# Optimization experiments

Hardware: AMD Instinct MI355X
Metric: run time of the kernel (lower is better)

Reference implementation:

```python
import jax, jax.numpy as jnp
import numpy as np

DIM = 2048
N_HEADS = 32
N_KV_HEADS = 4
HEAD_DIM = DIM // N_HEADS  # 64


def _rope_tables(T, head_dim, dtype):
    inv_freq = 1.0 / (10000.0 ** (jnp.arange(0, head_dim, 2, dtype=jnp.float32) / head_dim))
    t = jnp.arange(T, dtype=jnp.float32)
    freqs = jnp.einsum('i,j->ij', t, inv_freq)           # [T, head_dim/2]
    emb = jnp.concatenate([freqs, freqs], axis=-1)        # [T, head_dim]
    return jnp.cos(emb).astype(dtype), jnp.sin(emb).astype(dtype)


def _rotate_half(x):
    d = x.shape[-1] // 2
    return jnp.concatenate([-x[..., d:], x[..., :d]], axis=-1)


def setup_inputs() -> dict:
    key = jax.random.key(0)
    kx, kq, kk, kv, ko = jax.random.split(key, 5)
    s = 1.0 / np.sqrt(DIM)
    return {
        'x': jax.random.normal(kx, (2, 2048, DIM), dtype=jnp.float32),
        'wq': jax.random.normal(kq, (DIM, DIM), dtype=jnp.float32) * s,
        'wk': jax.random.normal(kk, (DIM, DIM // 8), dtype=jnp.float32) * s,
        'wv': jax.random.normal(kv, (DIM, DIM // 8), dtype=jnp.float32) * s,
        'wo': jax.random.normal(ko, (DIM, DIM), dtype=jnp.float32) * s,
    }


def reference(x, wq, wk, wv, wo):
    B, T, C = x.shape
    q = (x @ wq).reshape(B, T, N_HEADS, HEAD_DIM).transpose(0, 2, 1, 3)      # [B,H,T,D]
    k = (x @ wk).reshape(B, T, N_KV_HEADS, HEAD_DIM).transpose(0, 2, 1, 3)   # [B,Hkv,T,D]
    v = (x @ wv).reshape(B, T, N_KV_HEADS, HEAD_DIM).transpose(0, 2, 1, 3)

    cos, sin = _rope_tables(T, HEAD_DIM, x.dtype)  # [T,D]
    q = q * cos + _rotate_half(q) * sin
    k = k * cos + _rotate_half(k) * sin

    rep = N_HEADS // N_KV_HEADS
    k = jnp.repeat(k, rep, axis=1)  # [B,H,T,D]
    v = jnp.repeat(v, rep, axis=1)

    scale = 1.0 / np.sqrt(HEAD_DIM)
    scores = jnp.einsum('bhqd,bhkd->bhqk', q, k) * scale
    causal = jnp.tril(jnp.ones((T, T), dtype=bool))
    scores = jnp.where(causal, scores, jnp.finfo(scores.dtype).min)
    attn = jax.nn.softmax(scores, axis=-1)
    out = jnp.einsum('bhqk,bhkd->bhqd', attn, v)
    out = out.transpose(0, 2, 1, 3).reshape(B, T, C)
    return out @ wo
```

## Files before the change

kernel.cpp:

```cpp
#include <hip/hip_runtime.h>
#include <hip/hip_bf16.h>
#include <stdint.h>

#define DIM 2048
#define TSEQ 2048
#define BATCH 2
#define NH 32
#define NKV 4
#define HD 64
#define MROWS (BATCH*TSEQ)
#define NQKV 2560

typedef __attribute__((ext_vector_type(4))) float f32x4;
typedef __attribute__((ext_vector_type(8))) __bf16 bf16x8;
typedef unsigned short ushort_t;

#define GLDS16(g, l) __builtin_amdgcn_global_load_lds( \
    (const __attribute__((address_space(1))) void*)(g), \
    (__attribute__((address_space(3))) void*)(l), 16, 0, 0)

__device__ __forceinline__ float bflo2f(unsigned int w) {
  union { unsigned int i; float f; } c; c.i = w << 16; return c.f;
}
__device__ __forceinline__ unsigned short f2bf(float f) {
  union { float f; unsigned int i; } c; c.f = f;
  unsigned int x = c.i;
  x += 0x7fffu + ((x >> 16) & 1u);
  return (unsigned short)(x >> 16);
}
__device__ __forceinline__ unsigned short f2bf_fast(float f) {
  union { float f; unsigned int i; } c; c.f = f;
  return (unsigned short)((c.i + 0x8000u) >> 16);
}

__global__ void cast_bf16_k(const float* __restrict__ in, ushort_t* __restrict__ out, int n4) {
  const int i = blockIdx.x * 256 + threadIdx.x;
  if (i >= n4) return;
  const float4 v = ((const float4*)in)[i];
  uint2 p;
  p.x = (unsigned int)f2bf(v.x) | ((unsigned int)f2bf(v.y) << 16);
  p.y = (unsigned int)f2bf(v.z) | ((unsigned int)f2bf(v.w) << 16);
  ((uint2*)out)[i] = p;
}

__global__ void transpose_cast_all(const float* __restrict__ wq, const float* __restrict__ wk,
                                   const float* __restrict__ wv, const float* __restrict__ wo,
                                   ushort_t* __restrict__ wtq, ushort_t* __restrict__ woT) {
  __shared__ float tile[32][33];
  const int by = blockIdx.y;
  const float* src; ushort_t* dst; int N, bnb;
  if (by < 64)      { src = wq; dst = wtq;                    N = DIM; bnb = by; }
  else if (by < 72) { src = wk; dst = wtq + (long)DIM  * DIM; N = 256; bnb = by - 64; }
  else if (by < 80) { src = wv; dst = wtq + (long)2304 * DIM; N = 256; bnb = by - 72; }
  else              { src = wo; dst = woT;                    N = DIM; bnb = by - 80; }
  const int bk = blockIdx.x * 32;
  const int bn = bnb * 32;
  const int tx = threadIdx.x & 31;
  const int ty = threadIdx.x >> 5;
#pragma unroll
  for (int p = 0; p < 4; p++) {
    const int r = ty + p * 8;
    tile[r][tx] = src[(long)(bk + r) * N + bn + tx];
  }
  __syncthreads();
#pragma unroll
  for (int p = 0; p < 4; p++) {
    const int r = ty + p * 8;
    dst[(long)(bn + r) * DIM + bk + tx] = f2bf(tile[tx][r]);
  }
}

#define LOG1E4_D32 0.2878231366242557f
#define QSCALE 0.1803368801111243f

__global__ void rope_tab_k(float2* __restrict__ tab) {
  const int i = blockIdx.x * 256 + threadIdx.x;
  const int t = i >> 5, d = i & 31;
  const float ang = (float)t * __expf(-(float)d * LOG1E4_D32);
  float s_, c_;
  __sincosf(ang, &s_, &c_);
  tab[i] = make_float2(c_, s_);
}

template<int EPI>
__global__ __launch_bounds__(256, 4) void gemm_bt(
    const ushort_t* __restrict__ A, const ushort_t* __restrict__ BT,
    int M, int N, int K,
    float* __restrict__ Cf, ushort_t* __restrict__ Cq,
    ushort_t* __restrict__ Ck, ushort_t* __restrict__ Cv,
    const float2* __restrict__ tab)
{
  __shared__ __align__(16) ushort_t As[128][64];
  __shared__ __align__(16) ushort_t Bs[128][64];
  const int tid  = threadIdx.x;
  const int lane = tid & 63;
  const int wid  = tid >> 6;
  const int wm   = wid >> 1, wn = wid & 1;
  const int l8   = lane >> 3;
  const int c8   = (lane & 7) * 8;
  const long abase = (long)blockIdx.x * 128 * K;
  const long bbase = (long)blockIdx.y * 128 * K;
  const int rsel = lane & 15;
  const int koff = (lane >> 4) * 8;
  f32x4 acc[4][4] = {};

  for (int k0 = 0; k0 < K; k0 += 64) {
    __syncthreads();
#pragma unroll
    for (int i = 0; i < 4; i++) {
      const int r0 = wid * 32 + i * 8;
      GLDS16(&A [abase + (long)(r0 + l8) * K + k0 + c8], &As[r0][0]);
      GLDS16(&BT[bbase + (long)(r0 + l8) * K + k0 + c8], &Bs[r0][0]);
    }
    __syncthreads();
#pragma unroll
    for (int kk = 0; kk < 64; kk += 32) {
      bf16x8 af[4], bfr[4];
#pragma unroll
      for (int m = 0; m < 4; m++) af[m]  = *(const bf16x8*)(&As[wm*64 + m*16 + rsel][kk + koff]);
#pragma unroll
      for (int n = 0; n < 4; n++) bfr[n] = *(const bf16x8*)(&Bs[wn*64 + n*16 + rsel][kk + koff]);
#pragma unroll
      for (int m = 0; m < 4; m++)
#pragma unroll
        for (int n = 0; n < 4; n++)
          acc[m][n] = __builtin_amdgcn_mfma_f32_16x16x32_bf16(af[m], bfr[n], acc[m][n], 0, 0, 0);
    }
  }

  const int rbase = blockIdx.x * 128 + wm * 64 + (lane >> 4) * 4;
  const int l15e  = lane & 15;

  if (EPI == 1) {
    const int cbase = blockIdx.y * 128 + wn * 64 + l15e;
#pragma unroll
    for (int m = 0; m < 4; m++)
#pragma unroll
      for (int n = 0; n < 4; n++) {
        const int gn = cbase + n * 16;
#pragma unroll
        for (int j = 0; j < 4; j++)
          Cf[(long)(rbase + m * 16 + j) * N + gn] = acc[m][n][j];
      }
  } else {
    const int colbase = blockIdx.y * 128 + wn * 64;
    if (colbase >= DIM + 256) {
#pragma unroll
      for (int m = 0; m < 4; m++) {
        const int gm0 = rbase + m * 16;
        const int b = gm0 >> 11;
        const int t = gm0 & (TSEQ - 1);
#pragma unroll
        for (int n = 0; n < 4; n++) {
          const int x = colbase + n * 16 + l15e - DIM;
          const int hkv = (x >> 6) & 3;
          const int d = x & 63;
          uint2 pk;
          pk.x = (unsigned int)f2bf(acc[m][n][0]) | ((unsigned int)f2bf(acc[m][n][1]) << 16);
          pk.y = (unsigned int)f2bf(acc[m][n][2]) | ((unsigned int)f2bf(acc[m][n][3]) << 16);
          *(uint2*)(&Cv[((long)(b * NKV + hkv) * HD + d) * TSEQ + t]) = pk;
        }
      }
    } else {
      const bool isQ = (colbase < DIM);
      const int hkv = (colbase - DIM) >> 6;
#pragma unroll
      for (int m = 0; m < 4; m++) {
#pragma unroll
        for (int j = 0; j < 4; j++) {
          const int gm = rbase + m * 16 + j;
          const int t = gm & (TSEQ - 1);
          const int b = gm >> 11;
          const float2 cs0 = tab[t * 32 + l15e];
          const float2 cs1 = tab[t * 32 + 16 + l15e];
          const float v0 = acc[m][0][j], v1 = acc[m][1][j];
          const float v2 = acc[m][2][j], v3 = acc[m][3][j];
          const float r0 = v0 * cs0.x - v2 * cs0.y;
          const float r2 = v2 * cs0.x + v0 * cs0.y;
          const float r1 = v1 * cs1.x - v3 * cs1.y;
          const float r3 = v3 * cs1.x + v1 * cs1.y;
          if (isQ) {
            const long base = (long)gm * DIM + colbase + l15e;
            Cq[base]      = f2bf(r0 * QSCALE);
            Cq[base + 16] = f2bf(r1 * QSCALE);
            Cq[base + 32] = f2bf(r2 * QSCALE);
            Cq[base + 48] = f2bf(r3 * QSCALE);
          } else {
            const long base = ((long)(b * NKV + hkv) * TSEQ + t) * HD + l15e;
            Ck[base]      = f2bf(r0);
            Ck[base + 16] = f2bf(r1);
            Ck[base + 32] = f2bf(r2);
            Ck[base + 48] = f2bf(r3);
          }
        }
      }
    }
  }
}

__global__ __launch_bounds__(256, 4) void attn_mfma(
    const ushort_t* __restrict__ q, const ushort_t* __restrict__ k,
    const ushort_t* __restrict__ vt, ushort_t* __restrict__ o)
{
  __shared__ __align__(16) ushort_t Ks[2][64][64];
  __shared__ __align__(16) ushort_t Vs[2][64][64];

  const int tid  = threadIdx.x;
  const int lane = tid & 63;
  const int wid  = tid >> 6;
  const int l15  = lane & 15;
  const int lg   = lane >> 4;
  const int od   = lg & 1;
  const int hi   = lg >> 1;
  const int sw   = l15 & 7;

  const int bh  = blockIdx.x & 63;
  const int pq  = blockIdx.x >> 6;
  const int qtA = 31 - pq;
  const int qtB = pq;
  const int h   = bh & (NH - 1);
  const int b   = bh >> 5;
  const int hkv = h >> 3;
  const int qA0 = qtA * 64 + wid * 16;
  const int qB0 = qtB * 64 + wid * 16;

  bf16x8 qfA0, qfA1, qfB0, qfB1;
  {
    const ushort_t* qp = q + ((long)(b * TSEQ) + qA0 + l15) * DIM + h * 64 + lg * 8;
    qfA0 = *(const bf16x8*)(qp);
    qfA1 = *(const bf16x8*)(qp + 32);
    const ushort_t* qp2 = q + ((long)(b * TSEQ) + qB0 + l15) * DIM + h * 64 + lg * 8;
    qfB0 = *(const bf16x8*)(qp2);
    qfB1 = *(const bf16x8*)(qp2 + 32);
  }

  const ushort_t* kb_ = k  + (long)(b * NKV + hkv) * TSEQ * HD;
  const ushort_t* vb_ = vt + (long)(b * NKV + hkv) * HD * TSEQ;

  float lA = 0.f, lB = 0.f;
  f32x4 oA[4] = {}, oB[4] = {};

  const int srow = tid >> 2;
  const int sgc  = (tid & 3) * 16;
  const int g0   = 2 * (tid & 3);
  const int slc0 = ((g0    ) ^ (srow & 7)) * 8;
  const int slc1 = ((g0 + 1) ^ (srow & 7)) * 8;

  const int gv0 = ((0 + 2 * od + hi) ^ sw) * 8;
  const int gv1 = ((4 + 2 * od + hi) ^ sw) * 8;

  const int nkv = qtA + 1;

  *(uint4*)(&Ks[0][srow][slc0]) = *(const uint4*)(&kb_[(long)srow * HD + sgc]);
  *(uint4*)(&Ks[0][srow][slc1]) = *(const uint4*)(&kb_[(long)srow * HD + sgc + 8]);
  *(uint4*)(&Vs[0][srow][slc0]) = *(const uint4*)(&vb_[(long)srow * TSEQ + sgc]);
  *(uint4*)(&Vs[0][srow][slc1]) = *(const uint4*)(&vb_[(long)srow * TSEQ + sgc + 8]);
  int cur = 0;

#define PACK_KT(KT, UA, UB, LL) { \
    const float p0 = exp2f(st[KT][0]); \
    const float p1 = exp2f(st[KT][1]); \
    const float p2 = exp2f(st[KT][2]); \
    const float p3 = exp2f(st[KT][3]); \
    LL += (p0 + p1) + (p2 + p3); \
    asm("v_cvt_pk_bf16_f32 %0, %1, %2" : "=v"(UA) : "v"(p0), "v"(p1)); \
    asm("v_cvt_pk_bf16_f32 %0, %1, %2" : "=v"(UB) : "v"(p2), "v"(p3)); \
  }

#define PROC_TILE(QF0, QF1, OO, LL, Q0) \
  if (kb0 <= (Q0) + 15) { \
    f32x4 st[4] = {}; \
    __builtin_amdgcn_s_setprio(1); \
    _Pragma("unroll") \
    for (int kt = 0; kt < 4; kt++) { \
      const bf16x8 kf0 = *(const bf16x8*)(&Ks[cur][kt * 16 + l15][((0 + lg) ^ sw) * 8]); \
      st[kt] = __builtin_amdgcn_mfma_f32_16x16x32_bf16(kf0, QF0, st[kt], 0, 0, 0); \
      const bf16x8 kf1 = *(const bf16x8*)(&Ks[cur][kt * 16 + l15][((4 + lg) ^ sw) * 8]); \
      st[kt] = __builtin_amdgcn_mfma_f32_16x16x32_bf16(kf1, QF1, st[kt], 0, 0, 0); \
    } \
    __builtin_amdgcn_s_setprio(0); \
    if (kb0 + 63 > (Q0)) { \
      const int qg = (Q0) + l15; \
      _Pragma("unroll") \
      for (int kt = 0; kt < 4; kt++) { \
        const int kg0 = kb0 + kt * 16 + lg * 4; \
        _Pragma("unroll") \
        for (int j = 0; j < 4; j++) { \
          if (kg0 + j > qg) st[kt][j] = -1e30f; \
        } \
      } \
    } \
    unsigned int u00, u01, u10, u11, u20, u21, u30, u31; \
    PACK_KT(0, u00, u01, LL) \
    PACK_KT(1, u10, u11, LL) \
    PACK_KT(2, u20, u21, LL) \
    PACK_KT(3, u30, u31, LL) \
    const unsigned int r00 = __shfl_xor((int)(od ? u00 : u10), 16, 64); \
    const unsigned int r01 = __shfl_xor((int)(od ? u01 : u11), 16, 64); \
    const unsigned int r10 = __shfl_xor((int)(od ? u20 : u30), 16, 64); \
    const unsigned int r11 = __shfl_xor((int)(od ? u21 : u31), 16, 64); \
    union { unsigned int u[4]; bf16x8 v; } T0, T1; \
    T0.u[0] = od ? r00 : u00;  T0.u[1] = od ? r01 : u01; \
    T0.u[2] = od ? u10 : r00;  T0.u[3] = od ? u11 : r01; \
    T1.u[0] = od ? r10 : u20;  T1.u[1] = od ? r11 : u21; \
    T1.u[2] = od ? u30 : r10;  T1.u[3] = od ? u31 : r11; \
    __builtin_amdgcn_s_setprio(1); \
    _Pragma("unroll") \
    for (int nt = 0; nt < 4; nt++) { \
      const bf16x8 vf0 = *(const bf16x8*)(&Vs[cur][nt * 16 + l15][gv0]); \
      OO[nt] = __builtin_amdgcn_mfma_f32_16x16x32_bf16(T0.v, vf0, OO[nt], 0, 0, 0); \
    } \
    _Pragma("unroll") \
    for (int nt = 0; nt < 4; nt++) { \
      const bf16x8 vf1 = *(const bf16x8*)(&Vs[cur][nt * 16 + l15][gv1]); \
      OO[nt] = __builtin_amdgcn_mfma_f32_16x16x32_bf16(T1.v, vf1, OO[nt], 0, 0, 0); \
    } \
    __builtin_amdgcn_s_setprio(0); \
  }

  for (int kbv = 0; kbv < nkv; kbv++) {
    const int kb0 = kbv * 64;
    const bool pf = (kbv + 1 < nkv);
    uint4 kr0 = {}, kr1 = {}, vr0 = {}, vr1 = {};
    if (pf) {
      kr0 = *(const uint4*)(&kb_[(long)(kb0 + 64 + srow) * HD + sgc]);
      kr1 = *(const uint4*)(&kb_[(long)(kb0 + 64 + srow) * HD + sgc + 8]);
      vr0 = *(const uint4*)(&vb_[(long)srow * TSEQ + kb0 + 64 + sgc]);
      vr1 = *(const uint4*)(&vb_[(long)srow * TSEQ + kb0 + 64 + sgc + 8]);
    }
    asm volatile("s_waitcnt lgkmcnt(0)\n\ts_barrier" ::: "memory");

    PROC_TILE(qfA0, qfA1, oA, lA, qA0)
    PROC_TILE(qfB0, qfB1, oB, lB, qB0)

    if (pf) {
      *(uint4*)(&Ks[cur ^ 1][srow][slc0]) = kr0;
      *(uint4*)(&Ks[cur ^ 1][srow][slc1]) = kr1;
      *(uint4*)(&Vs[cur ^ 1][srow][slc0]) = vr0;
      *(uint4*)(&Vs[cur ^ 1][srow][slc1]) = vr1;
    }
    cur ^= 1;
  }
#undef PROC_TILE
#undef PACK_KT

  {
    float lc = lA;
    lc += __shfl_xor(lc, 16, 64);
    lc += __shfl_xor(lc, 32, 64);
    const long orow = (long)(b * TSEQ) + qA0;
#pragma unroll
    for (int j = 0; j < 4; j++) {
      const float inv = 1.f / __shfl(lc, (lane & 48) | (lg * 4 + j), 64);
#pragma unroll
      for (int nt = 0; nt < 4; nt++)
        o[(orow + lg * 4 + j) * DIM + h * 64 + nt * 16 + l15] = f2bf_fast(oA[nt][j] * inv);
    }
  }
  {
    float lc = lB;
    lc += __shfl_xor(lc, 16, 64);
    lc += __shfl_xor(lc, 32, 64);
    const long orow = (long)(b * TSEQ) + qB0;
#pragma unroll
    for (int j = 0; j < 4; j++) {
      const float inv = 1.f / __shfl(lc, (lane & 48) | (lg * 4 + j), 64);
#pragma unroll
      for (int nt = 0; nt < 4; nt++)
        o[(orow + lg * 4 + j) * DIM + h * 64 + nt * 16 + l15] = f2bf_fast(oB[nt][j] * inv);
    }
  }
}

extern "C" void kernel_launch(void* const* d_in, const int* in_sizes, int n_in,
                              void* d_out, int out_size, void* d_ws, size_t ws_size,
                              hipStream_t stream) {
  const float* x  = (const float*)d_in[0];
  const float* wq = (const float*)d_in[1];
  const float* wk = (const float*)d_in[2];
  const float* wv = (const float*)d_in[3];
  const float* wo = (const float*)d_in[4];
  float* out = (float*)d_out;

  ushort_t* ws = (ushort_t*)d_ws;
  const long NXB = (long)MROWS * DIM;
  ushort_t* xb   = ws;
  ushort_t* wtq  = xb  + NXB;
  ushort_t* woT  = wtq + (long)NQKV * DIM;
  ushort_t* qws  = woT + (long)DIM * DIM;
  ushort_t* kws  = qws + NXB;
  ushort_t* vtws = kws + (long)BATCH * NKV * TSEQ * HD;
  ushort_t* aws  = vtws + (long)BATCH * NKV * TSEQ * HD;
  float2*   tab  = (float2*)(aws + NXB);

  cast_bf16_k<<<(int)(NXB / 1024), 256, 0, stream>>>(x, xb, (int)(NXB / 4));
  transpose_cast_all<<<dim3(64, 144), 256, 0, stream>>>(wq, wk, wv, wo, wtq, woT);
  rope_tab_k<<<256, 256, 0, stream>>>(tab);

  gemm_bt<0><<<dim3(32, 20), 256, 0, stream>>>(xb, wtq, MROWS, NQKV, DIM,
                                               nullptr, qws, kws, vtws, tab);

  attn_mfma<<<BATCH * NH * 16, 256, 0, stream>>>(qws, kws, vtws, aws);

  gemm_bt<1><<<dim3(32, 16), 256, 0, stream>>>(aws, woT, MROWS, DIM, DIM,
                                               out, nullptr, nullptr, nullptr, nullptr);
}
```

Baseline: 203.3 us.

## Give each attention block one contiguous 128-row query tile so K/V fragments are shared

Each attention block now handles a single contiguous 128-row query tile, with each wave owning 32 consecutive rows, instead of pairing two 64-row tiles from opposite ends of the sequence. K and V fragments are loaded once from LDS into registers and reused for both 16-row halves of the wave, which halves LDS reads per MFMA. The K-loop now also skips fully masked tiles at the block level. The cost is higher register pressure, so launch bounds drop from 4 to 3 blocks per CU, and causal load balancing across blocks becomes uneven, now only mitigated by launching the longest tiles first.

```diff
diff --git a/kernel.cpp b/kernel.cpp
--- a/kernel.cpp
+++ b/kernel.cpp
@@ -198,7 +198,7 @@
   }
 }
 
-__global__ __launch_bounds__(256, 4) void attn_mfma(
+__global__ __launch_bounds__(256, 3) void attn_mfma(
     const ushort_t* __restrict__ q, const ushort_t* __restrict__ k,
     const ushort_t* __restrict__ vt, ushort_t* __restrict__ o)
 {
@@ -215,30 +215,27 @@
   const int sw   = l15 & 7;
 
   const int bh  = blockIdx.x & 63;
-  const int pq  = blockIdx.x >> 6;
-  const int qtA = 31 - pq;
-  const int qtB = pq;
+  const int qt  = (TSEQ / 128 - 1) - (blockIdx.x >> 6);
   const int h   = bh & (NH - 1);
   const int b   = bh >> 5;
   const int hkv = h >> 3;
-  const int qA0 = qtA * 64 + wid * 16;
-  const int qB0 = qtB * 64 + wid * 16;
-
-  bf16x8 qfA0, qfA1, qfB0, qfB1;
+  const int qw0 = qt * 128 + wid * 32;
+
+  bf16x8 qf0c0, qf0c1, qf1c0, qf1c1;
   {
-    const ushort_t* qp = q + ((long)(b * TSEQ) + qA0 + l15) * DIM + h * 64 + lg * 8;
-    qfA0 = *(const bf16x8*)(qp);
-    qfA1 = *(const bf16x8*)(qp + 32);
-    const ushort_t* qp2 = q + ((long)(b * TSEQ) + qB0 + l15) * DIM + h * 64 + lg * 8;
-    qfB0 = *(const bf16x8*)(qp2);
-    qfB1 = *(const bf16x8*)(qp2 + 32);
+    const ushort_t* qp0 = q + ((long)(b * TSEQ) + qw0 + l15) * DIM + h * 64 + lg * 8;
+    qf0c0 = *(const bf16x8*)(qp0);
+    qf0c1 = *(const bf16x8*)(qp0 + 32);
+    const ushort_t* qp1 = qp0 + 16 * DIM;
+    qf1c0 = *(const bf16x8*)(qp1);
+    qf1c1 = *(const bf16x8*)(qp1 + 32);
   }
 
   const ushort_t* kb_ = k  + (long)(b * NKV + hkv) * TSEQ * HD;
   const ushort_t* vb_ = vt + (long)(b * NKV + hkv) * HD * TSEQ;
 
-  float lA = 0.f, lB = 0.f;
-  f32x4 oA[4] = {}, oB[4] = {};
+  float lH0 = 0.f, lH1 = 0.f;
+  f32x4 oH0[4] = {}, oH1[4] = {};
 
   const int srow = tid >> 2;
   const int sgc  = (tid & 3) * 16;
@@ -249,7 +246,7 @@
   const int gv0 = ((0 + 2 * od + hi) ^ sw) * 8;
   const int gv1 = ((4 + 2 * od + hi) ^ sw) * 8;
 
-  const int nkv = qtA + 1;
+  const int nkv = 2 * qt + 2;
 
   *(uint4*)(&Ks[0][srow][slc0]) = *(const uint4*)(&kb_[(long)srow * HD + sgc]);
   *(uint4*)(&Ks[0][srow][slc1]) = *(const uint4*)(&kb_[(long)srow * HD + sgc + 8]);
@@ -257,65 +254,44 @@
   *(uint4*)(&Vs[0][srow][slc1]) = *(const uint4*)(&vb_[(long)srow * TSEQ + sgc + 8]);
   int cur = 0;
 
-#define PACK_KT(KT, UA, UB, LL) { \
-    const float p0 = exp2f(st[KT][0]); \
-    const float p1 = exp2f(st[KT][1]); \
-    const float p2 = exp2f(st[KT][2]); \
-    const float p3 = exp2f(st[KT][3]); \
+  union packu { unsigned int u[4]; bf16x8 v; };
+
+#define PK(ST, KT, UA, UB, LL) { \
+    const float p0 = exp2f(ST[KT][0]); \
+    const float p1 = exp2f(ST[KT][1]); \
+    const float p2 = exp2f(ST[KT][2]); \
+    const float p3 = exp2f(ST[KT][3]); \
     LL += (p0 + p1) + (p2 + p3); \
     asm("v_cvt_pk_bf16_f32 %0, %1, %2" : "=v"(UA) : "v"(p0), "v"(p1)); \
     asm("v_cvt_pk_bf16_f32 %0, %1, %2" : "=v"(UB) : "v"(p2), "v"(p3)); \
   }
 
-#define PROC_TILE(QF0, QF1, OO, LL, Q0) \
-  if (kb0 <= (Q0) + 15) { \
-    f32x4 st[4] = {}; \
-    __builtin_amdgcn_s_setprio(1); \
-    _Pragma("unroll") \
-    for (int kt = 0; kt < 4; kt++) { \
-      const bf16x8 kf0 = *(const bf16x8*)(&Ks[cur][kt * 16 + l15][((0 + lg) ^ sw) * 8]); \
-      st[kt] = __builtin_amdgcn_mfma_f32_16x16x32_bf16(kf0, QF0, st[kt], 0, 0, 0); \
-      const bf16x8 kf1 = *(const bf16x8*)(&Ks[cur][kt * 16 + l15][((4 + lg) ^ sw) * 8]); \
-      st[kt] = __builtin_amdgcn_mfma_f32_16x16x32_bf16(kf1, QF1, st[kt], 0, 0, 0); \
-    } \
-    __builtin_amdgcn_s_setprio(0); \
-    if (kb0 + 63 > (Q0)) { \
-      const int qg = (Q0) + l15; \
-      _Pragma("unroll") \
-      for (int kt = 0; kt < 4; kt++) { \
-        const int kg0 = kb0 + kt * 16 + lg * 4; \
-        _Pragma("unroll") \
-        for (int j = 0; j < 4; j++) { \
-          if (kg0 + j > qg) st[kt][j] = -1e30f; \
-        } \
-      } \
-    } \
+#define PACK_HALF(ST, LL, TT0, TT1) { \
     unsigned int u00, u01, u10, u11, u20, u21, u30, u31; \
-    PACK_KT(0, u00, u01, LL) \
-    PACK_KT(1, u10, u11, LL) \
-    PACK_KT(2, u20, u21, LL) \
-    PACK_KT(3, u30, u31, LL) \
+    PK(ST, 0, u00, u01, LL) \
+    PK(ST, 1, u10, u11, LL) \
+    PK(ST, 2, u20, u21, LL) \
+    PK(ST, 3, u30, u31, LL) \
     const unsigned int r00 = __shfl_xor((int)(od ? u00 : u10), 16, 64); \
     const unsigned int r01 = __shfl_xor((int)(od ? u01 : u11), 16, 64); \
     const unsigned int r10 = __shfl_xor((int)(od ? u20 : u30), 16, 64); \
     const unsigned int r11 = __shfl_xor((int)(od ? u21 : u31), 16, 64); \
-    union { unsigned int u[4]; bf16x8 v; } T0, T1; \
-    T0.u[0] = od ? r00 : u00;  T0.u[1] = od ? r01 : u01; \
-    T0.u[2] = od ? u10 : r00;  T0.u[3] = od ? u11 : r01; \
-    T1.u[0] = od ? r10 : u20;  T1.u[1] = od ? r11 : u21; \
-    T1.u[2] = od ? u30 : r10;  T1.u[3] = od ? u31 : r11; \
-    __builtin_amdgcn_s_setprio(1); \
+    TT0.u[0] = od ? r00 : u00;  TT0.u[1] = od ? r01 : u01; \
+    TT0.u[2] = od ? u10 : r00;  TT0.u[3] = od ? u11 : r01; \
+    TT1.u[0] = od ? r10 : u20;  TT1.u[1] = od ? r11 : u21; \
+    TT1.u[2] = od ? u30 : r10;  TT1.u[3] = od ? u31 : r11; \
+  }
+
+#define MASK_ST(ST, Q0) { \
+    const int qg = (Q0) + l15; \
     _Pragma("unroll") \
-    for (int nt = 0; nt < 4; nt++) { \
-      const bf16x8 vf0 = *(const bf16x8*)(&Vs[cur][nt * 16 + l15][gv0]); \
-      OO[nt] = __builtin_amdgcn_mfma_f32_16x16x32_bf16(T0.v, vf0, OO[nt], 0, 0, 0); \
+    for (int kt = 0; kt < 4; kt++) { \
+      const int kg0 = kb0 + kt * 16 + lg * 4; \
+      _Pragma("unroll") \
+      for (int j = 0; j < 4; j++) { \
+        if (kg0 + j > qg) ST[kt][j] = -1e30f; \
+      } \
     } \
-    _Pragma("unroll") \
-    for (int nt = 0; nt < 4; nt++) { \
-      const bf16x8 vf1 = *(const bf16x8*)(&Vs[cur][nt * 16 + l15][gv1]); \
-      OO[nt] = __builtin_amdgcn_mfma_f32_16x16x32_bf16(T1.v, vf1, OO[nt], 0, 0, 0); \
-    } \
-    __builtin_amdgcn_s_setprio(0); \
   }
 
   for (int kbv = 0; kbv < nkv; kbv++) {
@@ -330,8 +306,69 @@
     }
     asm volatile("s_waitcnt lgkmcnt(0)\n\ts_barrier" ::: "memory");
 
-    PROC_TILE(qfA0, qfA1, oA, lA, qA0)
-    PROC_TILE(qfB0, qfB1, oB, lB, qB0)
+    const bool a1 = (kb0 <= qw0 + 31);
+    if (a1) {
+      const bool a0 = (kb0 <= qw0 + 15);
+
+      bf16x8 kfa[4], kfb[4];
+#pragma unroll
+      for (int kt = 0; kt < 4; kt++) {
+        kfa[kt] = *(const bf16x8*)(&Ks[cur][kt * 16 + l15][((0 + lg) ^ sw) * 8]);
+        kfb[kt] = *(const bf16x8*)(&Ks[cur][kt * 16 + l15][((4 + lg) ^ sw) * 8]);
+      }
+
+      f32x4 st1[4] = {};
+      __builtin_amdgcn_s_setprio(1);
+#pragma unroll
+      for (int kt = 0; kt < 4; kt++) {
+        st1[kt] = __builtin_amdgcn_mfma_f32_16x16x32_bf16(kfa[kt], qf1c0, st1[kt], 0, 0, 0);
+        st1[kt] = __builtin_amdgcn_mfma_f32_16x16x32_bf16(kfb[kt], qf1c1, st1[kt], 0, 0, 0);
+      }
+      __builtin_amdgcn_s_setprio(0);
+      f32x4 st0[4] = {};
+      if (a0) {
+        __builtin_amdgcn_s_setprio(1);
+#pragma unroll
+        for (int kt = 0; kt < 4; kt++) {
+          st0[kt] = __builtin_amdgcn_mfma_f32_16x16x32_bf16(kfa[kt], qf0c0, st0[kt], 0, 0, 0);
+          st0[kt] = __builtin_amdgcn_mfma_f32_16x16x32_bf16(kfb[kt], qf0c1, st0[kt], 0, 0, 0);
+        }
+        __builtin_amdgcn_s_setprio(0);
+      }
+
+      if (kb0 + 63 > qw0 + 16) MASK_ST(st1, qw0 + 16)
+      if (a0 && kb0 + 63 > qw0) MASK_ST(st0, qw0)
+
+      packu T0H1, T1H1, T0H0, T1H0;
+      PACK_HALF(st1, lH1, T0H1, T1H1)
+      if (a0) PACK_HALF(st0, lH0, T0H0, T1H0)
+
+      bf16x8 vfa[4], vfb[4];
+#pragma unroll
+      for (int nt = 0; nt < 4; nt++) {
+        vfa[nt] = *(const bf16x8*)(&Vs[cur][nt * 16 + l15][gv0]);
+        vfb[nt] = *(const bf16x8*)(&Vs[cur][nt * 16 + l15][gv1]);
+      }
+
+      __builtin_amdgcn_s_setprio(1);
+#pragma unroll
+      for (int nt = 0; nt < 4; nt++)
+        oH1[nt] = __builtin_amdgcn_mfma_f32_16x16x32_bf16(T0H1.v, vfa[nt], oH1[nt], 0, 0, 0);
+#pragma unroll
+      for (int nt = 0; nt < 4; nt++)
+        oH1[nt] = __builtin_amdgcn_mfma_f32_16x16x32_bf16(T1H1.v, vfb[nt], oH1[nt], 0, 0, 0);
+      __builtin_amdgcn_s_setprio(0);
+      if (a0) {
+        __builtin_amdgcn_s_setprio(1);
+#pragma unroll
+        for (int nt = 0; nt < 4; nt++)
+          oH0[nt] = __builtin_amdgcn_mfma_f32_16x16x32_bf16(T0H0.v, vfa[nt], oH0[nt], 0, 0, 0);
+#pragma unroll
+        for (int nt = 0; nt < 4; nt++)
+          oH0[nt] = __builtin_amdgcn_mfma_f32_16x16x32_bf16(T1H0.v, vfb[nt], oH0[nt], 0, 0, 0);
+        __builtin_amdgcn_s_setprio(0);
+      }
+    }
 
     if (pf) {
       *(uint4*)(&Ks[cur ^ 1][srow][slc0]) = kr0;
@@ -341,33 +378,34 @@
     }
     cur ^= 1;
   }
-#undef PROC_TILE
-#undef PACK_KT
+#undef MASK_ST
+#undef PACK_HALF
+#undef PK
 
   {
-    float lc = lA;
+    float lc = lH0;
     lc += __shfl_xor(lc, 16, 64);
     lc += __shfl_xor(lc, 32, 64);
-    const long orow = (long)(b * TSEQ) + qA0;
+    const long orow = (long)(b * TSEQ) + qw0;
 #pragma unroll
     for (int j = 0; j < 4; j++) {
       const float inv = 1.f / __shfl(lc, (lane & 48) | (lg * 4 + j), 64);
 #pragma unroll
       for (int nt = 0; nt < 4; nt++)
-        o[(orow + lg * 4 + j) * DIM + h * 64 + nt * 16 + l15] = f2bf_fast(oA[nt][j] * inv);
+        o[(orow + lg * 4 + j) * DIM + h * 64 + nt * 16 + l15] = f2bf_fast(oH0[nt][j] * inv);
     }
   }
   {
-    float lc = lB;
+    float lc = lH1;
     lc += __shfl_xor(lc, 16, 64);
     lc += __shfl_xor(lc, 32, 64);
-    const long orow = (long)(b * TSEQ) + qB0;
+    const long orow = (long)(b * TSEQ) + qw0 + 16;
 #pragma unroll
     for (int j = 0; j < 4; j++) {
       const float inv = 1.f / __shfl(lc, (lane & 48) | (lg * 4 + j), 64);
 #pragma unroll
       for (int nt = 0; nt < 4; nt++)
-        o[(orow + lg * 4 + j) * DIM + h * 64 + nt * 16 + l15] = f2bf_fast(oB[nt][j] * inv);
+        o[(orow + lg * 4 + j) * DIM + h * 64 + nt * 16 + l15] = f2bf_fast(oH1[nt][j] * inv);
     }
   }
 }
@@ -400,7 +438,7 @@
   gemm_bt<0><<<dim3(32, 20), 256, 0, stream>>>(xb, wtq, MROWS, NQKV, DIM,
                                                nullptr, qws, kws, vtws, tab);
 
-  attn_mfma<<<BATCH * NH * 16, 256, 0, stream>>>(qws, kws, vtws, aws);
+  attn_mfma<<<BATCH * NH * (TSEQ / 128), 256, 0, stream>>>(qws, kws, vtws, aws);
 
   gemm_bt<1><<<dim3(32, 16), 256, 0, stream>>>(aws, woT, MROWS, DIM, DIM,
                                                out, nullptr, nullptr, nullptr, nullptr);
```

New measurement: 202.0 us. No clear change (-0.6%).
